# Kernel tuning notes

Measured on AMD Instinct MI355X. Metric: run time of the kernel, lower is better.

The kernel has to match this reference:

```python
import jax, jax.numpy as jnp
import numpy as np

N_EMBD = 1024  # C; source scales scores by C**-0.5 (n_embd, not head_size)


def setup_inputs() -> dict:
    key = jax.random.key(0)
    kx, kk, kq, kv = jax.random.split(key, 4)
    B, T, C, H = 8, 2048, N_EMBD, 64
    x = jax.random.normal(kx, (B, T, C), dtype=jnp.float32)
    Wk = jax.random.normal(kk, (C, H), dtype=jnp.float32) * (C ** -0.5)
    Wq = jax.random.normal(kq, (C, H), dtype=jnp.float32) * (C ** -0.5)
    Wv = jax.random.normal(kv, (C, H), dtype=jnp.float32) * (C ** -0.5)
    return {"x": x, "Wk": Wk, "Wq": Wq, "Wv": Wv}


def reference(x, Wk, Wq, Wv):
    B, T, C = x.shape
    k = jnp.einsum('btc,ch->bth', x, Wk)
    q = jnp.einsum('btc,ch->bth', x, Wq)
    v = jnp.einsum('btc,ch->bth', x, Wv)
    # scores scaled by C**-0.5 (faithful to source, which uses n_embd not head_size)
    wei = jnp.einsum('bth,bsh->bts', q, k) * (C ** -0.5)  # [B,T,T]
    causal = jnp.tril(jnp.ones((T, T), dtype=bool))
    wei = jnp.where(causal, wei, -jnp.inf)
    wei = jax.nn.softmax(wei, axis=-1)
    # dropout is identity in eval mode
    out = jnp.einsum('bts,bsh->bth', wei, v)
    return out
```

## Files before the change

### kernel.cpp

```cpp
#include <hip/hip_runtime.h>


#define B_ 8
#define T_ 2048
#define C_ 1024
#define H_ 64
#define BTH (B_ * T_ * H_)

typedef unsigned short u16;
typedef float f32x4 __attribute__((ext_vector_type(4)));
typedef __bf16 bf16x8 __attribute__((ext_vector_type(8)));
#define AS1 __attribute__((address_space(1)))
#define AS3 __attribute__((address_space(3)))

__device__ __forceinline__ u16 f2bf(float f) {
  union { float f; unsigned u; } c; c.f = f;
  unsigned u = c.u;
  return (u16)((u + 0x7FFFu + ((u >> 16) & 1u)) >> 16);
}

__device__ __forceinline__ bf16x8 cvt8(const float4 a, const float4 b) {
  bf16x8 r;
  r[0] = (__bf16)a.x; r[1] = (__bf16)a.y; r[2] = (__bf16)a.z; r[3] = (__bf16)a.w;
  r[4] = (__bf16)b.x; r[5] = (__bf16)b.y; r[6] = (__bf16)b.z; r[7] = (__bf16)b.w;
  return r;
}

__global__ __launch_bounds__(256)
void wpack(const float* __restrict__ Wk, const float* __restrict__ Wq,
           const float* __restrict__ Wv, u16* __restrict__ Wct) {
  const int g  = blockIdx.x;
  const int k0 = blockIdx.y * 64;
  const float* __restrict__ W = (g == 0) ? Wk : (g == 1) ? Wq : Wv;
#pragma unroll
  for (int it = 0; it < 16; ++it) {
    const int idx = it * 256 + threadIdx.x;
    const int kk = k0 + (idx >> 6), h = idx & 63;
    Wct[(size_t)(g * 64 + h) * C_ + kk] = f2bf(W[(size_t)kk * H_ + h]);
  }
}

__global__ __launch_bounds__(256)
void qkv_gemm(const float* __restrict__ x, const u16* __restrict__ Wct,
              u16* __restrict__ ws) {
  __shared__ u16 As[32 * 128];
  const int tid  = threadIdx.x;
  const int wave = tid >> 6, lane = tid & 63;
  const int l15 = lane & 15, quad = lane >> 4;
  const int r0 = blockIdx.x * 32;
  const int srow = tid >> 3, sseg = tid & 7;
  const float* __restrict__ xsrc = x + (size_t)(r0 + srow) * C_ + sseg * 16;
  u16* const wdst0 = As + srow * 128 + ((2 * sseg)     ^ (srow & 15)) * 8;
  u16* const wdst1 = As + srow * 128 + ((2 * sseg + 1) ^ (srow & 15)) * 8;
  const u16* __restrict__ wp = Wct + (size_t)(wave * 48 + l15) * C_ + quad * 8;
  const u16* const ard0 = As + l15 * 128;
  const u16* const ard1 = As + (16 + l15) * 128;
  const f32x4 z = {0.f, 0.f, 0.f, 0.f};
  f32x4 acc[2][3];
#pragma unroll
  for (int m = 0; m < 2; ++m)
#pragma unroll
    for (int ni = 0; ni < 3; ++ni) acc[m][ni] = z;

#pragma unroll 1
  for (int ks = 0; ks < 8; ++ks) {
    const int k0 = ks * 128;
    float4 xa0 = *(const float4*)(xsrc + k0);
    float4 xa1 = *(const float4*)(xsrc + k0 + 4);
    float4 xa2 = *(const float4*)(xsrc + k0 + 8);
    float4 xa3 = *(const float4*)(xsrc + k0 + 12);
    bf16x8 Bf[3][4];
#pragma unroll
    for (int ni = 0; ni < 3; ++ni)
#pragma unroll
      for (int f = 0; f < 4; ++f)
        Bf[ni][f] = *(const bf16x8*)(wp + (size_t)ni * 16 * C_ + k0 + f * 32);
    __syncthreads();
    *(bf16x8*)wdst0 = cvt8(xa0, xa1);
    *(bf16x8*)wdst1 = cvt8(xa2, xa3);
    __syncthreads();
#pragma unroll
    for (int f = 0; f < 4; ++f) {
      const int co = (((4 * f + quad) ^ l15) * 8);
      const bf16x8 a0 = *(const bf16x8*)(ard0 + co);
      const bf16x8 a1 = *(const bf16x8*)(ard1 + co);
#pragma unroll
      for (int ni = 0; ni < 3; ++ni) {
        acc[0][ni] = __builtin_amdgcn_mfma_f32_16x16x32_bf16(a0, Bf[ni][f], acc[0][ni], 0, 0, 0);
        acc[1][ni] = __builtin_amdgcn_mfma_f32_16x16x32_bf16(a1, Bf[ni][f], acc[1][ni], 0, 0, 0);
      }
    }
  }
  const float SCLL = 0.03125f * 1.44269504088896f;
  const int bb = r0 >> 11;
#pragma unroll
  for (int m = 0; m < 2; ++m) {
    const int rowg = r0 + m * 16;
    const int tb = (rowg & 2047) + quad * 4;
#pragma unroll
    for (int ni = 0; ni < 3; ++ni) {
      const int col = wave * 48 + ni * 16 + l15;
      const int g = col >> 6, h = col & 63;
      f32x4 a = acc[m][ni];
      if (g == 1) { a[0] *= SCLL; a[1] *= SCLL; a[2] *= SCLL; a[3] *= SCLL; }
      if (g < 2) {
        u16* op = ws + (size_t)g * BTH + (size_t)(rowg + quad * 4) * H_ + h;
#pragma unroll
        for (int r = 0; r < 4; ++r) op[(size_t)r * H_] = f2bf(a[r]);
      } else {
        uint2 pk;
        pk.x = (unsigned)f2bf(a[0]) | ((unsigned)f2bf(a[1]) << 16);
        pk.y = (unsigned)f2bf(a[2]) | ((unsigned)f2bf(a[3]) << 16);
        *(uint2*)(ws + (size_t)2 * BTH + (size_t)(bb * H_ + h) * T_ + tb) = pk;
      }
    }
  }
}

__global__ __launch_bounds__(256)
void flash(const u16* __restrict__ ws, float* __restrict__ fpart) {
  __shared__ u16 Ks[2][64 * 64];
  __shared__ u16 Vs[2][64 * 64];
  __shared__ __bf16 Pt[4][16 * 72];
  const u16* __restrict__ kg = ws;
  const u16* __restrict__ qg = ws + BTH;
  const u16* __restrict__ vt = ws + (size_t)2 * BTH;
  const int b  = blockIdx.y;
  const int bx = 143 - (int)blockIdx.x;
  int c = 0;
#pragma unroll
  for (int t = 1; t < 8; ++t)
    if (34 * t - 2 * t * t <= bx) c = t;
  const int u = 4 * c + (bx - (34 * c - 2 * c * c));
  const int tid  = threadIdx.x;
  const int wv   = tid >> 6;
  const int lane = tid & 63;
  const int l15  = lane & 15, quad = lane >> 4;
  const int qt   = 4 * u + wv;
  const int t0   = qt * 16;
  const int st0  = 4 * c;
  const int stE  = (st0 + 4 < u + 1) ? st0 + 4 : u + 1;
  const u16* kb0 = kg + (size_t)b * T_ * H_;
  const u16* vb0 = vt + (size_t)b * H_ * T_;
  const int srow = tid >> 3, scp = tid & 7;
  const u16* qrow = qg + ((size_t)(b * T_ + t0 + l15)) * H_ + quad * 8;
  const bf16x8 qf0 = *(const bf16x8*)qrow;
  const bf16x8 qf1 = *(const bf16x8*)(qrow + 32);
  __bf16* pt = &Pt[wv][0];
  const f32x4 z = {0.f, 0.f, 0.f, 0.f};
  f32x4 o[4];
  float lr[4] = {0.f, 0.f, 0.f, 0.f};
#pragma unroll
  for (int hi = 0; hi < 4; ++hi) o[hi] = z;

  {
    const int s00 = st0 * 64;
#pragma unroll
    for (int jj = 0; jj < 2; ++jj) {
      const int row = jj * 32 + srow;
      const int sc  = scp ^ (row & 7);
      __builtin_amdgcn_global_load_lds(
          (const AS1 unsigned*)(kb0 + (size_t)(s00 + row) * H_ + sc * 8),
          (AS3 unsigned*)(&Ks[0][(jj * 256 + tid) * 8]), 16, 0, 0);
      __builtin_amdgcn_global_load_lds(
          (const AS1 unsigned*)(vb0 + (size_t)row * T_ + s00 + sc * 8),
          (AS3 unsigned*)(&Vs[0][(jj * 256 + tid) * 8]), 16, 0, 0);
    }
  }
  __syncthreads();

#pragma unroll 1
  for (int st = st0; st < stE; ++st) {
    const int cur = (st - st0) & 1;
    if (st + 1 < stE) {
      const int s1 = (st + 1) * 64;
#pragma unroll
      for (int jj = 0; jj < 2; ++jj) {
        const int row = jj * 32 + srow;
        const int sc  = scp ^ (row & 7);
        __builtin_amdgcn_global_load_lds(
            (const AS1 unsigned*)(kb0 + (size_t)(s1 + row) * H_ + sc * 8),
            (AS3 unsigned*)(&Ks[cur ^ 1][(jj * 256 + tid) * 8]), 16, 0, 0);
        __builtin_amdgcn_global_load_lds(
            (const AS1 unsigned*)(vb0 + (size_t)row * T_ + s1 + sc * 8),
            (AS3 unsigned*)(&Vs[cur ^ 1][(jj * 256 + tid) * 8]), 16, 0, 0);
      }
    }
    const u16* Kc = &Ks[cur][0];
    const u16* Vc = &Vs[cur][0];
    const int sw = (l15 & 7);
    f32x4 s[4];
#pragma unroll
    for (int ni = 0; ni < 4; ++ni) {
      const u16* kr = Kc + (ni * 16 + l15) * 64;
      const bf16x8 k0 = *(const bf16x8*)(kr + ((quad       ^ sw) * 8));
      const bf16x8 k1 = *(const bf16x8*)(kr + (((4 + quad) ^ sw) * 8));
      s[ni] = __builtin_amdgcn_mfma_f32_16x16x32_bf16(qf0, k0, z, 0, 0, 0);
      s[ni] = __builtin_amdgcn_mfma_f32_16x16x32_bf16(qf1, k1, s[ni], 0, 0, 0);
    }
    if (st == u) {
      const int s0 = st * 64;
#pragma unroll
      for (int ni = 0; ni < 4; ++ni)
#pragma unroll
        for (int r = 0; r < 4; ++r)
          if (s0 + ni * 16 + l15 > t0 + quad * 4 + r) s[ni][r] = -1e30f;
    }
    float p[4][4];
#pragma unroll
    for (int ni = 0; ni < 4; ++ni)
#pragma unroll
      for (int r = 0; r < 4; ++r) p[ni][r] = __builtin_amdgcn_exp2f(s[ni][r]);
#pragma unroll
    for (int r = 0; r < 4; ++r)
      lr[r] += (p[0][r] + p[1][r]) + (p[2][r] + p[3][r]);
#pragma unroll
    for (int ni = 0; ni < 4; ++ni)
#pragma unroll
      for (int r = 0; r < 4; ++r)
        pt[(quad * 4 + r) * 72 + ni * 16 + l15] = (__bf16)p[ni][r];
    asm volatile("s_waitcnt lgkmcnt(0)" ::: "memory");
    const bf16x8 pa0 = *(const bf16x8*)(pt + l15 * 72 + quad * 8);
    const bf16x8 pa1 = *(const bf16x8*)(pt + l15 * 72 + 32 + quad * 8);
    asm volatile("" ::: "memory");
#pragma unroll
    for (int hi = 0; hi < 4; ++hi) {
      const u16* vr = Vc + (hi * 16 + l15) * 64;
      const bf16x8 v0 = *(const bf16x8*)(vr + ((quad       ^ sw) * 8));
      const bf16x8 v1 = *(const bf16x8*)(vr + (((4 + quad) ^ sw) * 8));
      o[hi] = __builtin_amdgcn_mfma_f32_16x16x32_bf16(pa0, v0, o[hi], 0, 0, 0);
      o[hi] = __builtin_amdgcn_mfma_f32_16x16x32_bf16(pa1, v1, o[hi], 0, 0, 0);
    }
    __syncthreads();
  }
#pragma unroll
  for (int d = 1; d < 16; d <<= 1)
#pragma unroll
    for (int r = 0; r < 4; ++r) lr[r] += __shfl_xor(lr[r], d, 64);
  float* po = fpart + (size_t)((b * 128 + qt) * 8 + c) * 1040;
#pragma unroll
  for (int hi = 0; hi < 4; ++hi)
#pragma unroll
    for (int r = 0; r < 4; ++r)
      po[(quad * 4 + r) * 64 + hi * 16 + l15] = o[hi][r];
  if (l15 == 0) {
#pragma unroll
    for (int r = 0; r < 4; ++r) po[1024 + quad * 4 + r] = lr[r];
  }
}

__global__ __launch_bounds__(256)
void freduce(const float* __restrict__ fpart, float* __restrict__ out) {
  const int qt  = blockIdx.x;
  const int b   = blockIdx.y;
  const int tid = threadIdx.x;
  const int nc  = (qt >> 4) + 1;
  const float* __restrict__ pb = fpart + (size_t)(b * 128 + qt) * 8 * 1040;
  __shared__ float ls[16];
  if (tid < 16) {
    float s = 0.f;
#pragma unroll 1
    for (int i = 0; i < nc; ++i) s += pb[(size_t)i * 1040 + 1024 + tid];
    ls[tid] = s;
  }
  __syncthreads();
  f32x4 a = {0.f, 0.f, 0.f, 0.f};
#pragma unroll 1
  for (int i = 0; i < nc; ++i)
    a += *(const f32x4*)(pb + (size_t)i * 1040 + tid * 4);
  const float inv = 1.0f / ls[tid >> 4];
  a[0] *= inv; a[1] *= inv; a[2] *= inv; a[3] *= inv;
  *(f32x4*)(out + (size_t)(b * T_ + qt * 16 + (tid >> 4)) * H_ + ((tid * 4) & 63)) = a;
}

extern "C" void kernel_launch(void* const* d_in, const int* in_sizes, int n_in,
                              void* d_out, int out_size, void* d_ws, size_t ws_size,
                              hipStream_t stream) {
  const float* x  = (const float*)d_in[0];
  const float* Wk = (const float*)d_in[1];
  const float* Wq = (const float*)d_in[2];
  const float* Wv = (const float*)d_in[3];
  u16*   ws  = (u16*)d_ws;
  u16*   Wct = ws + (size_t)3 * BTH;
  float* fpart = (float*)(ws + (size_t)3 * BTH + 192 * 1024);
  float* out = (float*)d_out;
  wpack<<<dim3(3, 16), 256, 0, stream>>>(Wk, Wq, Wv, Wct);
  qkv_gemm<<<dim3(512), 256, 0, stream>>>(x, Wct, ws);
  flash<<<dim3(144, B_), 256, 0, stream>>>(ws, fpart);
  freduce<<<dim3(128, B_), 256, 0, stream>>>(fpart, out);
}
```

Measured before the change: 142.9 us.

## Stage QKV weight tiles in LDS via async global_load_lds with register-prefetched x

Reworks the QKV projection GEMM so that weight tiles (192x64 bf16) are loaded straight into shared memory with global_load_lds rather than streamed per-wave into registers from global memory. The K loop now uses 64-wide steps with a swizzled LDS layout, and the next x tile is prefetched into registers while MFMAs run on the current one. It also adds an occupancy hint of 5 blocks per CU. This aims to cut register pressure and redundant global weight reads. In exchange it adds LDS traffic, runs twice as many K iterations, and uses single-buffered LDS with two barriers per step.

Result: faster. 137.3 us (-3.9%).

```diff
diff --git a/kernel.cpp b/kernel.cpp
--- a/kernel.cpp
+++ b/kernel.cpp
@@ -40,21 +40,19 @@
   }
 }
 
-__global__ __launch_bounds__(256)
+__global__ __launch_bounds__(256, 5)
 void qkv_gemm(const float* __restrict__ x, const u16* __restrict__ Wct,
               u16* __restrict__ ws) {
-  __shared__ u16 As[32 * 128];
+  __shared__ u16 Bs[192 * 64];
+  __shared__ u16 Xs[32 * 64];
   const int tid  = threadIdx.x;
-  const int wave = tid >> 6, lane = tid & 63;
+  const int wv   = tid >> 6, lane = tid & 63;
   const int l15 = lane & 15, quad = lane >> 4;
   const int r0 = blockIdx.x * 32;
-  const int srow = tid >> 3, sseg = tid & 7;
-  const float* __restrict__ xsrc = x + (size_t)(r0 + srow) * C_ + sseg * 16;
-  u16* const wdst0 = As + srow * 128 + ((2 * sseg)     ^ (srow & 15)) * 8;
-  u16* const wdst1 = As + srow * 128 + ((2 * sseg + 1) ^ (srow & 15)) * 8;
-  const u16* __restrict__ wp = Wct + (size_t)(wave * 48 + l15) * C_ + quad * 8;
-  const u16* const ard0 = As + l15 * 128;
-  const u16* const ard1 = As + (16 + l15) * 128;
+  const int xrow = tid >> 3, xcp = tid & 7;
+  const float* __restrict__ xsrc = x + (size_t)(r0 + xrow) * C_ + xcp * 8;
+  u16* const xdst = &Xs[xrow * 64 + ((xcp ^ (xrow & 7)) * 8)];
+  const int cksw = l15 & 7;
   const f32x4 z = {0.f, 0.f, 0.f, 0.f};
   f32x4 acc[2][3];
 #pragma unroll
@@ -62,44 +60,62 @@
 #pragma unroll
     for (int ni = 0; ni < 3; ++ni) acc[m][ni] = z;
 
+  float4 xr0 = *(const float4*)(xsrc);
+  float4 xr1 = *(const float4*)(xsrc + 4);
+#pragma unroll
+  for (int it = 0; it < 6; ++it) {
+    const int slot = it * 256 + tid;
+    const int row = slot >> 3, cp = slot & 7;
+    __builtin_amdgcn_global_load_lds(
+        (const AS1 unsigned*)(Wct + (size_t)row * C_ + ((cp ^ (row & 7)) * 8)),
+        (AS3 unsigned*)(&Bs[slot * 8]), 16, 0, 0);
+  }
+  *(bf16x8*)xdst = cvt8(xr0, xr1);
+  __syncthreads();
+
 #pragma unroll 1
-  for (int ks = 0; ks < 8; ++ks) {
-    const int k0 = ks * 128;
-    float4 xa0 = *(const float4*)(xsrc + k0);
-    float4 xa1 = *(const float4*)(xsrc + k0 + 4);
-    float4 xa2 = *(const float4*)(xsrc + k0 + 8);
-    float4 xa3 = *(const float4*)(xsrc + k0 + 12);
-    bf16x8 Bf[3][4];
-#pragma unroll
-    for (int ni = 0; ni < 3; ++ni)
-#pragma unroll
-      for (int f = 0; f < 4; ++f)
-        Bf[ni][f] = *(const bf16x8*)(wp + (size_t)ni * 16 * C_ + k0 + f * 32);
+  for (int st = 0; st < 16; ++st) {
+    if (st < 15) {
+      xr0 = *(const float4*)(xsrc + (st + 1) * 64);
+      xr1 = *(const float4*)(xsrc + (st + 1) * 64 + 4);
+    }
+#pragma unroll
+    for (int kk = 0; kk < 2; ++kk) {
+      const int co = ((kk * 4 + quad) ^ cksw) * 8;
+      const bf16x8 a0 = *(const bf16x8*)(&Xs[l15 * 64 + co]);
+      const bf16x8 a1 = *(const bf16x8*)(&Xs[(16 + l15) * 64 + co]);
+#pragma unroll
+      for (int ni = 0; ni < 3; ++ni) {
+        const bf16x8 b = *(const bf16x8*)(&Bs[(wv * 48 + ni * 16 + l15) * 64 + co]);
+        acc[0][ni] = __builtin_amdgcn_mfma_f32_16x16x32_bf16(a0, b, acc[0][ni], 0, 0, 0);
+        acc[1][ni] = __builtin_amdgcn_mfma_f32_16x16x32_bf16(a1, b, acc[1][ni], 0, 0, 0);
+      }
+    }
     __syncthreads();
-    *(bf16x8*)wdst0 = cvt8(xa0, xa1);
-    *(bf16x8*)wdst1 = cvt8(xa2, xa3);
+    if (st < 15) {
+      const int k1 = (st + 1) * 64;
+#pragma unroll
+      for (int it = 0; it < 6; ++it) {
+        const int slot = it * 256 + tid;
+        const int row = slot >> 3, cp = slot & 7;
+        __builtin_amdgcn_global_load_lds(
+            (const AS1 unsigned*)(Wct + (size_t)row * C_ + k1 + ((cp ^ (row & 7)) * 8)),
+            (AS3 unsigned*)(&Bs[slot * 8]), 16, 0, 0);
+      }
+      *(bf16x8*)xdst = cvt8(xr0, xr1);
+    }
     __syncthreads();
-#pragma unroll
-    for (int f = 0; f < 4; ++f) {
-      const int co = (((4 * f + quad) ^ l15) * 8);
-      const bf16x8 a0 = *(const bf16x8*)(ard0 + co);
-      const bf16x8 a1 = *(const bf16x8*)(ard1 + co);
-#pragma unroll
-      for (int ni = 0; ni < 3; ++ni) {
-        acc[0][ni] = __builtin_amdgcn_mfma_f32_16x16x32_bf16(a0, Bf[ni][f], acc[0][ni], 0, 0, 0);
-        acc[1][ni] = __builtin_amdgcn_mfma_f32_16x16x32_bf16(a1, Bf[ni][f], acc[1][ni], 0, 0, 0);
-      }
-    }
-  }
+  }
+
   const float SCLL = 0.03125f * 1.44269504088896f;
-  const int bb = r0 >> 11;
 #pragma unroll
   for (int m = 0; m < 2; ++m) {
     const int rowg = r0 + m * 16;
+    const int bb = rowg >> 11;
     const int tb = (rowg & 2047) + quad * 4;
 #pragma unroll
     for (int ni = 0; ni < 3; ++ni) {
-      const int col = wave * 48 + ni * 16 + l15;
+      const int col = wv * 48 + ni * 16 + l15;
       const int g = col >> 6, h = col & 63;
       f32x4 a = acc[m][ni];
       if (g == 1) { a[0] *= SCLL; a[1] *= SCLL; a[2] *= SCLL; a[3] *= SCLL; }
```
